# Kernel tuning notes

Measured on AMD Instinct MI355X. Metric: run time of the kernel, lower is better.

Reference implementation:

```python
import jax, jax.numpy as jnp
import numpy as np

KEEP_RATIO = 0.3
ALPHA, BETA, GAMMA, SMOOTH = 0.3, 0.7, 1.33, 1e-6
LOVASZ_W = 0.2


def _bce_with_logits(x, t):
    # stable binary_cross_entropy_with_logits, reduction='none'
    return jnp.maximum(x, 0.0) - x * t + jnp.log1p(jnp.exp(-jnp.abs(x)))


def _ohem_image(loss_i, tgt_i, tis_i, k_all):
    # loss_i/tgt_i/tis_i: [P] per-image flattened
    P = loss_i.shape[0]
    pos = tgt_i * tis_i                       # 1.0 where kept positive
    n_pos = jnp.sum(pos).astype(jnp.int32)
    neg_mask = (tgt_i == 0) & (tis_i == 1)
    n_remain = jnp.maximum(0, k_all - n_pos)
    # top-n_remain negative losses via full descending sort + rank mask
    neg_vals = jnp.where(neg_mask, loss_i, -jnp.inf)
    neg_sorted = -jnp.sort(-neg_vals)         # descending
    ranks = jnp.arange(P)
    valid = (ranks < n_remain) & jnp.isfinite(neg_sorted)
    neg_sum = jnp.sum(jnp.where(valid, neg_sorted, 0.0))
    n_neg_kept = jnp.sum(valid).astype(jnp.int32)
    pos_sum = jnp.sum(loss_i * pos)
    cnt = n_pos + n_neg_kept
    # fallback when nothing kept: hardest pixel inside tissue (or pixel 0)
    tis_vals = jnp.where(tis_i == 1, loss_i, -jnp.inf)
    has_tissue = jnp.any(tis_i == 1)
    fallback = jnp.where(has_tissue, jnp.max(tis_vals), loss_i[0])
    return jnp.where(cnt > 0, (pos_sum + neg_sum) / jnp.maximum(cnt, 1), fallback)


def _lovasz_image(log_flat, lab_flat):
    # binary Lovasz hinge, per image
    signs = 2.0 * lab_flat - 1.0
    errors = 1.0 - log_flat * signs
    order = jnp.argsort(-errors)              # descending by error
    errors_sorted = errors[order]
    gt_sorted = lab_flat[order]
    p = jnp.sum(gt_sorted)
    intersection = p - jnp.cumsum(gt_sorted)
    union = p + jnp.cumsum(1.0 - gt_sorted)
    jaccard = 1.0 - intersection / union
    n = gt_sorted.shape[0] - p
    grad = jnp.where(n > 0,
                     jnp.concatenate([jaccard[:1], jaccard[1:] - jaccard[:-1]]),
                     jaccard)
    return jnp.dot(jax.nn.relu(errors_sorted), grad)


def _forward(logits, targets, tissue_mask):
    t = targets.astype(jnp.float32)
    B = logits.shape[0]
    lf = logits.reshape(B, -1)                # [B, P]
    tf = t.reshape(B, -1)
    mf = tissue_mask.reshape(B, -1)
    P = lf.shape[1]
    k_all = max(1, int(P * KEEP_RATIO))       # static

    # --- OHEM BCE ---
    bce = _bce_with_logits(lf, tf) * mf
    ohem_i = jax.vmap(lambda l, tg, ms: _ohem_image(l, tg, ms, k_all))(bce, tf, mf)
    ohem_term = jnp.mean(ohem_i)

    # --- focal Tversky (per image) ---
    probs = jax.nn.sigmoid(lf)
    tp = jnp.sum(probs * tf, axis=1)
    fn = jnp.sum((1.0 - probs) * tf, axis=1)
    fp = jnp.sum(probs * (1.0 - tf), axis=1)
    tversky = (tp + SMOOTH) / (tp + ALPHA * fn + BETA * fp + SMOOTH)
    ft_i = (1.0 - tversky) ** GAMMA

    # --- Lovasz hinge (per image) ---
    lov_i = jax.vmap(_lovasz_image)(lf, tf)

    # masked mean over images that contain positives
    posb = jnp.sum(tf, axis=1) > 0
    npos = jnp.sum(posb)
    denom = jnp.maximum(npos, 1).astype(lf.dtype)
    ft_term = jnp.sum(jnp.where(posb, ft_i, 0.0)) / denom
    lov_term = jnp.sum(jnp.where(posb, lov_i, 0.0)) / denom
    return ohem_term + jnp.where(npos > 0, ft_term + LOVASZ_W * lov_term, 0.0)


def setup_inputs() -> dict:
    key = jax.random.key(0)
    k1, k2 = jax.random.split(key)
    B, H, W = 16, 768, 768
    logits = jax.random.normal(k1, (B, 1, H, W), dtype=jnp.float32)
    targets = jax.random.randint(k2, (B, 1, H, W), 0, 2, dtype=jnp.int32)
    tissue_mask = jnp.ones((B, 1, H, W), dtype=jnp.float32)
    return {"logits": logits, "targets": targets, "tissue_mask": tissue_mask}


def reference(logits, targets, tissue_mask):
    return _forward(logits, targets, tissue_mask)
```

## Files before the change

### kernel.cpp

```cpp
#include <hip/hip_runtime.h>
#include <math.h>

#define BB 16
#define PP (768*768)
#define NBINS 4096
#define CHUNKS 96
#define KALL 176947

#define LOV_LO (-17.0f)
#define LOV_RANGE 34.0f

typedef unsigned long long u64;

struct PAcc { float pos_sum, pos_w, tpx, sprx, mx, sum_t, n_tis, bce0; };
struct AccR { float lov_i, ft_i, ohem_i; unsigned posb; };

__device__ inline float wred_sum(float v) {
  #pragma unroll
  for (int o = 32; o > 0; o >>= 1) v += __shfl_down(v, o, 64);
  return v;
}
__device__ inline float wred_max(float v) {
  #pragma unroll
  for (int o = 32; o > 0; o >>= 1) v = fmaxf(v, __shfl_down(v, o, 64));
  return v;
}

__global__ __launch_bounds__(256) void k_main(const float* __restrict__ logits,
                                              const int* __restrict__ targets,
                                              const float* __restrict__ mask,
                                              PAcc* __restrict__ pacc,
                                              unsigned* __restrict__ partial1,
                                              unsigned* __restrict__ partial3)
{
  const int b = blockIdx.y;
  const int chunk = blockIdx.x;
  __shared__ unsigned hist1[NBINS];
  __shared__ unsigned hist3p[NBINS / 2];
  __shared__ float wsum[4][8];
  for (int i = threadIdx.x; i < NBINS; i += 256) hist1[i] = 0u;
  for (int i = threadIdx.x; i < NBINS / 2; i += 256) hist3p[i] = 0u;
  __syncthreads();

  const float4* l4 = (const float4*)(logits + (size_t)b * PP);
  const int4*   t4 = (const int4*)(targets + (size_t)b * PP);
  const float4* m4 = (const float4*)(mask + (size_t)b * PP);

  const float lov_scale = (float)NBINS / LOV_RANGE;

  float pos_sum = 0.f, pos_w = 0.f, tpa = 0.f, spra = 0.f, mx = 0.f;
  float sum_t = 0.f, n_tis = 0.f, bce0 = 0.f;

  if (chunk == 0 && threadIdx.x == 0) {
    float l = logits[(size_t)b * PP];
    float tf = (float)targets[(size_t)b * PP];
    float m = mask[(size_t)b * PP];
    float ex = __expf(-fabsf(l));
    bce0 = (fmaxf(l, 0.f) + __logf(1.f + ex) - l * tf) * m;
  }

  const int per_chunk4 = (PP / CHUNKS) / 4;
  const int base4 = chunk * per_chunk4;
  const int iters = per_chunk4 / 256;

  for (int it = 0; it < iters; ++it) {
    int i = base4 + it * 256 + threadIdx.x;
    float4 lv = l4[i]; int4 tv = t4[i]; float4 mv = m4[i];
    float ls[4] = {lv.x, lv.y, lv.z, lv.w};
    int   ts[4] = {tv.x, tv.y, tv.z, tv.w};
    float ms[4] = {mv.x, mv.y, mv.z, mv.w};
    #pragma unroll
    for (int c = 0; c < 4; ++c) {
      float l = ls[c]; int ti = ts[c]; float tf = (float)ti; float m = ms[c];
      float ex = __expf(-fabsf(l));
      float lg = __logf(1.f + ex);
      float loss = (fmaxf(l, 0.f) + lg - l * tf) * m;
      float posw = tf * m;
      pos_sum = fmaf(loss, posw, pos_sum);
      pos_w  += posw;
      float pr = ((l >= 0.f) ? 1.f : ex) * __builtin_amdgcn_rcpf(1.f + ex);
      spra += pr;
      tpa = fmaf(pr, tf, tpa);
      sum_t += tf;
      bool tis = (m == 1.0f);
      if (tis) { n_tis += 1.f; mx = fmaxf(mx, loss); }
      float s = fmaf(2.f, tf, -1.f);
      float e = fmaf(-l, s, 1.f);
      int bin = (int)((e - LOV_LO) * lov_scale);
      bin = bin < 0 ? 0 : (bin > NBINS - 1 ? NBINS - 1 : bin);
      atomicAdd(&hist1[bin], 1u | ((unsigned)ti << 16));
      if ((ti == 0) & !tis)
        atomicAdd(&hist3p[bin >> 1], 1u << ((bin & 1) << 4));
    }
  }

  {
    float v0 = wred_sum(pos_sum), v1 = wred_sum(pos_w), v2 = wred_sum(tpa);
    float v3 = wred_sum(spra), v4 = wred_max(mx), v5 = wred_sum(sum_t);
    float v6 = wred_sum(n_tis), v7 = wred_sum(bce0);
    int w = threadIdx.x >> 6, lane = threadIdx.x & 63;
    if (lane == 0) {
      wsum[w][0] = v0; wsum[w][1] = v1; wsum[w][2] = v2; wsum[w][3] = v3;
      wsum[w][4] = v4; wsum[w][5] = v5; wsum[w][6] = v6; wsum[w][7] = v7;
    }
  }
  __syncthreads();
  if (threadIdx.x == 0) {
    PAcc r;
    r.pos_sum = wsum[0][0] + wsum[1][0] + wsum[2][0] + wsum[3][0];
    r.pos_w   = wsum[0][1] + wsum[1][1] + wsum[2][1] + wsum[3][1];
    r.tpx     = wsum[0][2] + wsum[1][2] + wsum[2][2] + wsum[3][2];
    r.sprx    = wsum[0][3] + wsum[1][3] + wsum[2][3] + wsum[3][3];
    r.mx      = fmaxf(fmaxf(wsum[0][4], wsum[1][4]), fmaxf(wsum[2][4], wsum[3][4]));
    r.sum_t   = wsum[0][5] + wsum[1][5] + wsum[2][5] + wsum[3][5];
    r.n_tis   = wsum[0][6] + wsum[1][6] + wsum[2][6] + wsum[3][6];
    r.bce0    = wsum[0][7] + wsum[1][7] + wsum[2][7] + wsum[3][7];
    pacc[(size_t)b * CHUNKS + chunk] = r;
  }

  {
    unsigned* d1 = partial1 + ((size_t)b * CHUNKS + chunk) * NBINS;
    for (int i = threadIdx.x; i < NBINS; i += 256) d1[i] = hist1[i];
    unsigned* d3 = partial3 + ((size_t)b * CHUNKS + chunk) * (NBINS / 2);
    for (int i = threadIdx.x; i < NBINS / 2; i += 256) d3[i] = hist3p[i];
  }
}

__global__ __launch_bounds__(256) void k_reduce(const unsigned* __restrict__ partial1,
                                                const unsigned* __restrict__ partial3,
                                                u64* __restrict__ ghist,
                                                const PAcc* __restrict__ pacc,
                                                PAcc* __restrict__ accImg,
                                                unsigned* __restrict__ ticket)
{
  const int img = blockIdx.y;
  const int slice = blockIdx.x;
  const int bin = slice * 256 + threadIdx.x;
  const unsigned* s1 = partial1 + (size_t)img * CHUNKS * NBINS + bin;
  const unsigned* s3 = partial3 + (size_t)img * CHUNKS * (NBINS / 2) + (bin >> 1);
  const unsigned sh3 = (bin & 1) << 4;
  unsigned c = 0, q = 0, n0 = 0;
  #pragma unroll 4
  for (int p = 0; p < CHUNKS; ++p) {
    unsigned v = s1[(size_t)p * NBINS];
    c += v & 0xFFFFu; q += v >> 16;
    n0 += (s3[(size_t)p * (NBINS / 2)] >> sh3) & 0xFFFFu;
  }
  unsigned negtis = (c - q) - n0;
  ghist[(size_t)img * NBINS + bin] =
      (u64)c | ((u64)q << 20) | ((u64)negtis << 40);

  if (slice == 0 && threadIdx.x < 128) {
    int t = threadIdx.x;
    PAcc v;
    if (t < CHUNKS) v = pacc[(size_t)img * CHUNKS + t];
    else { v.pos_sum = v.pos_w = v.tpx = v.sprx = v.mx = v.sum_t = v.n_tis = v.bce0 = 0.f; }
    v.pos_sum = wred_sum(v.pos_sum); v.pos_w = wred_sum(v.pos_w);
    v.tpx = wred_sum(v.tpx); v.sprx = wred_sum(v.sprx);
    v.mx = wred_max(v.mx); v.sum_t = wred_sum(v.sum_t);
    v.n_tis = wred_sum(v.n_tis); v.bce0 = wred_sum(v.bce0);
    __shared__ PAcc half[2];
    if ((t & 63) == 0) half[t >> 6] = v;
    __syncthreads();
    if (t == 0) {
      PAcc r = half[0], h = half[1];
      r.pos_sum += h.pos_sum; r.pos_w += h.pos_w; r.tpx += h.tpx; r.sprx += h.sprx;
      r.mx = fmaxf(r.mx, h.mx); r.sum_t += h.sum_t; r.n_tis += h.n_tis; r.bce0 += h.bce0;
      accImg[img] = r;
    }
  }
  if (slice == 0 && img == 0 && threadIdx.x == 0) *ticket = 0u;
}

__global__ __launch_bounds__(256) void k_scan(const PAcc* __restrict__ accImg,
                                              const u64* __restrict__ ghist,
                                              AccR* __restrict__ acc,
                                              unsigned* __restrict__ ticket,
                                              float* __restrict__ out)
{
  const int b = blockIdx.x;
  const int t = threadIdx.x;
  __shared__ unsigned sA[256], sB[256], sC[256];
  __shared__ float sf[256], sg[256];
  __shared__ unsigned ng_total_sh;

  const u64* gh = ghist + (size_t)b * NBINS;
  const PAcc a = accImg[b];

  const unsigned sum_t = (unsigned)a.sum_t;
  const float p = (float)sum_t;
  const bool has_pos = sum_t > 0;
  const unsigned n_neg_total = (unsigned)PP - sum_t;
  const int CH = NBINS / 256;
  const float lov_d = LOV_RANGE / (float)NBINS;

  int n_pos = (int)a.pos_w;
  int n_remain = KALL - n_pos; if (n_remain < 0) n_remain = 0;

  u64 loc[16];
  unsigned tc = 0, tq = 0, tn = 0;
  #pragma unroll
  for (int k = 0; k < 16; ++k) {
    u64 v = gh[NBINS - 1 - (t * CH + k)];
    loc[k] = v;
    tc += (unsigned)(v & 0xFFFFFu);
    tq += (unsigned)((v >> 20) & 0xFFFFFu);
    tn += (unsigned)((v >> 40) & 0xFFFFFu);
  }
  sA[t] = tc; sB[t] = tq; sC[t] = tn;
  __syncthreads();
  if (t == 0) {
    unsigned aI = 0, aC = 0, aN = 0;
    for (int i = 0; i < 256; i++) {
      unsigned ci = sA[i], qi = sB[i], ni = sC[i];
      sA[i] = aI; sB[i] = aC; sC[i] = aN;
      aI += ci; aC += qi; aN += ni;
    }
    ng_total_sh = aN;
  }
  __syncthreads();

  float lov_local = 0.f, ns_local = 0.f;
  {
    unsigned I = sA[t], C = sB[t], NG = sC[t];
    float Jprev = has_pos ? (1.f - (p - (float)C) / (p + (float)I - (float)C)) : 0.f;
    #pragma unroll 4
    for (int k = 0; k < 16; ++k) {
      int j = NBINS - 1 - (t * CH + k);
      u64 v = loc[k];
      unsigned c = (unsigned)(v & 0xFFFFFu);
      if (c) {
        unsigned q = (unsigned)((v >> 20) & 0xFFFFFu);
        unsigned ng = (unsigned)((v >> 40) & 0xFFFFFu);
        float e = LOV_LO + ((float)j + 0.5f) * lov_d;
        if (has_pos) {
          float re = fmaxf(e, 0.f);
          if (n_neg_total > 0) {
            I += c; C += q;
            float Jb = 1.f - (p - (float)C) / (p + (float)I - (float)C);
            lov_local += re * (Jb - Jprev);
            Jprev = Jb;
          } else {
            double hi = (double)I + (double)c;
            double s = (hi * (hi + 1.0) - (double)I * ((double)I + 1.0)) * 0.5 / (double)p;
            lov_local += re * (float)s;
            I += c;
          }
        }
        if (n_remain > 0 && ng) {
          long long rem = (long long)n_remain - (long long)NG;
          unsigned take = rem <= 0 ? 0u : (rem >= (long long)ng ? ng : (unsigned)rem);
          if (take) {
            float l = e - 1.f;
            float nloss = fmaxf(l, 0.f) + __logf(1.f + __expf(-fabsf(l)));
            ns_local += (float)take * nloss;
          }
          NG += ng;
        }
      }
    }
  }
  sf[t] = lov_local; sg[t] = ns_local; __syncthreads();
  for (int off = 128; off > 0; off >>= 1) {
    if (t < off) { sf[t] += sf[t + off]; sg[t] += sg[t + off]; }
    __syncthreads();
  }

  if (t == 0) {
    float lov = sf[0];
    float neg_sum = sg[0];
    unsigned kept = (n_remain > 0)
        ? ((unsigned)n_remain < ng_total_sh ? (unsigned)n_remain : ng_total_sh) : 0u;
    float cnt = (float)n_pos + (float)kept;
    float ohem;
    if (cnt > 0.f) ohem = (a.pos_sum + neg_sum) / cnt;
    else ohem = (a.n_tis > 0.f) ? a.mx : a.bce0;
    float tp = a.tpx;
    float fn = p - tp;
    float fp = a.sprx - tp;
    float tv = (tp + 1e-6f) / (tp + 0.3f * fn + 0.7f * fp + 1e-6f);
    float ft = powf(fmaxf(1.f - tv, 0.f), 1.33f);
    acc[b].lov_i = lov; acc[b].ft_i = ft; acc[b].ohem_i = ohem;
    acc[b].posb = has_pos ? 1u : 0u;

    __threadfence();
    unsigned ret = atomicAdd(ticket, 1u);
    if (ret == BB - 1) {
      __threadfence();
      volatile AccR* va = acc;
      float os = 0.f, fts = 0.f, lvs = 0.f; int np = 0;
      for (int i = 0; i < BB; i++) {
        os += va[i].ohem_i;
        if (va[i].posb) { np++; fts += va[i].ft_i; lvs += va[i].lov_i; }
      }
      float denom = (np > 0) ? (float)np : 1.f;
      float r = os / (float)BB;
      if (np > 0) r += fts / denom + 0.2f * (lvs / denom);
      out[0] = r;
    }
  }
}

extern "C" void kernel_launch(void* const* d_in, const int* in_sizes, int n_in,
                              void* d_out, int out_size, void* d_ws, size_t ws_size,
                              hipStream_t stream) {
  const float* logits  = (const float*)d_in[0];
  const int*   targets = (const int*)d_in[1];
  const float* mask    = (const float*)d_in[2];
  float* out = (float*)d_out;

  char* ws = (char*)d_ws;
  AccR*     acc      = (AccR*)ws;
  unsigned* ticket   = (unsigned*)(ws + 256);
  PAcc*     accImg   = (PAcc*)(ws + 512);
  PAcc*     pacc     = (PAcc*)(ws + 1024);
  u64*      ghist    = (u64*)(ws + (64 << 10));
  unsigned* partial1 = (unsigned*)(ws + (1 << 20));
  unsigned* partial3 = (unsigned*)(ws + (1 << 20) + (size_t)BB * CHUNKS * NBINS * 4);
  (void)in_sizes; (void)n_in; (void)out_size; (void)ws_size;


  dim3 g1(CHUNKS, BB, 1);
  k_main<<<g1, 256, 0, stream>>>(logits, targets, mask, pacc, partial1, partial3);
  dim3 g2(NBINS / 256, BB, 1);
  k_reduce<<<g2, 256, 0, stream>>>(partial1, partial3, ghist, pacc, accImg, ticket);
  k_scan<<<BB, 256, 0, stream>>>(accImg, ghist, acc, ticket, out);
}
```

Baseline: 170.9 us.

## Fuse reduce and scan kernels, skip unused negative-tissue histograms

Merges the reduce and scan kernels into one tail kernel. A per-image ticket picks the last slice block to run the scan, which removes one launch and the gap between them. k_main now writes a per-chunk flag saying whether any non-tissue pixels exist. It skips storing hist3p when the flag is clear, and the tail kernel skips reading it. It also unrolls the main loop two float4 groups at a time and adds an occupancy hint to launch_bounds. The cost is more ticket and fence synchronisation, and extra register pressure from the wider loads.

After: 198.0 us. +15.9%, slower.

```diff
diff --git a/kernel.cpp b/kernel.cpp
--- a/kernel.cpp
+++ b/kernel.cpp
@@ -5,6 +5,7 @@
 #define PP (768*768)
 #define NBINS 4096
 #define CHUNKS 96
+#define PIXB (PP / CHUNKS)
 #define KALL 176947
 
 #define LOV_LO (-17.0f)
@@ -26,20 +27,24 @@
   return v;
 }
 
-__global__ __launch_bounds__(256) void k_main(const float* __restrict__ logits,
-                                              const int* __restrict__ targets,
-                                              const float* __restrict__ mask,
-                                              PAcc* __restrict__ pacc,
-                                              unsigned* __restrict__ partial1,
-                                              unsigned* __restrict__ partial3)
+__global__ __launch_bounds__(256, 6) void k_main(const float* __restrict__ logits,
+                                                 const int* __restrict__ targets,
+                                                 const float* __restrict__ mask,
+                                                 PAcc* __restrict__ pacc,
+                                                 unsigned* __restrict__ partial1,
+                                                 unsigned* __restrict__ partial3,
+                                                 unsigned* __restrict__ flags,
+                                                 unsigned* __restrict__ tickets)
 {
   const int b = blockIdx.y;
   const int chunk = blockIdx.x;
   __shared__ unsigned hist1[NBINS];
   __shared__ unsigned hist3p[NBINS / 2];
   __shared__ float wsum[4][8];
+  __shared__ unsigned s_any3;
   for (int i = threadIdx.x; i < NBINS; i += 256) hist1[i] = 0u;
   for (int i = threadIdx.x; i < NBINS / 2; i += 256) hist3p[i] = 0u;
+  if (b == 0 && chunk == 0 && threadIdx.x < 17) tickets[threadIdx.x] = 0u;
   __syncthreads();
 
   const float4* l4 = (const float4*)(logits + (size_t)b * PP);
@@ -59,39 +64,45 @@
     bce0 = (fmaxf(l, 0.f) + __logf(1.f + ex) - l * tf) * m;
   }
 
-  const int per_chunk4 = (PP / CHUNKS) / 4;
+  auto px = [&](float l, int ti, float m) {
+    float tf = (float)ti;
+    float ex = __expf(-fabsf(l));
+    float lg = __logf(1.f + ex);
+    float loss = (fmaxf(l, 0.f) + lg - l * tf) * m;
+    float posw = tf * m;
+    pos_sum = fmaf(loss, posw, pos_sum);
+    pos_w  += posw;
+    float pr = ((l >= 0.f) ? 1.f : ex) * __builtin_amdgcn_rcpf(1.f + ex);
+    spra += pr;
+    tpa = fmaf(pr, tf, tpa);
+    sum_t += tf;
+    bool tis = (m == 1.0f);
+    if (tis) { n_tis += 1.f; mx = fmaxf(mx, loss); }
+    float s = fmaf(2.f, tf, -1.f);
+    float e = fmaf(-l, s, 1.f);
+    int bin = (int)((e - LOV_LO) * lov_scale);
+    bin = bin < 0 ? 0 : (bin > NBINS - 1 ? NBINS - 1 : bin);
+    atomicAdd(&hist1[bin], 1u | ((unsigned)ti << 16));
+    if ((ti == 0) & !tis)
+      atomicAdd(&hist3p[bin >> 1], 1u << ((bin & 1) << 4));
+  };
+  auto grp = [&](float4 lv, int4 tv, float4 mv) {
+    px(lv.x, tv.x, mv.x); px(lv.y, tv.y, mv.y);
+    px(lv.z, tv.z, mv.z); px(lv.w, tv.w, mv.w);
+  };
+
+  const int per_chunk4 = PIXB / 4;
   const int base4 = chunk * per_chunk4;
   const int iters = per_chunk4 / 256;
 
-  for (int it = 0; it < iters; ++it) {
-    int i = base4 + it * 256 + threadIdx.x;
-    float4 lv = l4[i]; int4 tv = t4[i]; float4 mv = m4[i];
-    float ls[4] = {lv.x, lv.y, lv.z, lv.w};
-    int   ts[4] = {tv.x, tv.y, tv.z, tv.w};
-    float ms[4] = {mv.x, mv.y, mv.z, mv.w};
-    #pragma unroll
-    for (int c = 0; c < 4; ++c) {
-      float l = ls[c]; int ti = ts[c]; float tf = (float)ti; float m = ms[c];
-      float ex = __expf(-fabsf(l));
-      float lg = __logf(1.f + ex);
-      float loss = (fmaxf(l, 0.f) + lg - l * tf) * m;
-      float posw = tf * m;
-      pos_sum = fmaf(loss, posw, pos_sum);
-      pos_w  += posw;
-      float pr = ((l >= 0.f) ? 1.f : ex) * __builtin_amdgcn_rcpf(1.f + ex);
-      spra += pr;
-      tpa = fmaf(pr, tf, tpa);
-      sum_t += tf;
-      bool tis = (m == 1.0f);
-      if (tis) { n_tis += 1.f; mx = fmaxf(mx, loss); }
-      float s = fmaf(2.f, tf, -1.f);
-      float e = fmaf(-l, s, 1.f);
-      int bin = (int)((e - LOV_LO) * lov_scale);
-      bin = bin < 0 ? 0 : (bin > NBINS - 1 ? NBINS - 1 : bin);
-      atomicAdd(&hist1[bin], 1u | ((unsigned)ti << 16));
-      if ((ti == 0) & !tis)
-        atomicAdd(&hist3p[bin >> 1], 1u << ((bin & 1) << 4));
-    }
+  for (int it = 0; it < iters; it += 2) {
+    int ia = base4 + it * 256 + threadIdx.x;
+    int ib = ia + 256;
+    float4 lva = l4[ia]; float4 lvb = l4[ib];
+    int4   tva = t4[ia]; int4   tvb = t4[ib];
+    float4 mva = m4[ia]; float4 mvb = m4[ib];
+    grp(lva, tva, mva);
+    grp(lvb, tvb, mvb);
   }
 
   {
@@ -116,76 +127,90 @@
     r.n_tis   = wsum[0][6] + wsum[1][6] + wsum[2][6] + wsum[3][6];
     r.bce0    = wsum[0][7] + wsum[1][7] + wsum[2][7] + wsum[3][7];
     pacc[(size_t)b * CHUNKS + chunk] = r;
-  }
+    unsigned any3 = (r.n_tis != (float)PIXB) ? 1u : 0u;
+    s_any3 = any3;
+    flags[(size_t)b * CHUNKS + chunk] = any3;
+  }
+  __syncthreads();
 
   {
     unsigned* d1 = partial1 + ((size_t)b * CHUNKS + chunk) * NBINS;
     for (int i = threadIdx.x; i < NBINS; i += 256) d1[i] = hist1[i];
-    unsigned* d3 = partial3 + ((size_t)b * CHUNKS + chunk) * (NBINS / 2);
-    for (int i = threadIdx.x; i < NBINS / 2; i += 256) d3[i] = hist3p[i];
-  }
-}
-
-__global__ __launch_bounds__(256) void k_reduce(const unsigned* __restrict__ partial1,
-                                                const unsigned* __restrict__ partial3,
-                                                u64* __restrict__ ghist,
-                                                const PAcc* __restrict__ pacc,
-                                                PAcc* __restrict__ accImg,
-                                                unsigned* __restrict__ ticket)
+    if (s_any3) {
+      unsigned* d3 = partial3 + ((size_t)b * CHUNKS + chunk) * (NBINS / 2);
+      for (int i = threadIdx.x; i < NBINS / 2; i += 256) d3[i] = hist3p[i];
+    }
+  }
+}
+
+__global__ __launch_bounds__(256) void k_tail(const unsigned* __restrict__ partial1,
+                                              const unsigned* __restrict__ partial3,
+                                              const unsigned* __restrict__ flags,
+                                              u64* __restrict__ ghist,
+                                              const PAcc* __restrict__ pacc,
+                                              PAcc* __restrict__ accImg,
+                                              AccR* __restrict__ acc,
+                                              unsigned* __restrict__ tickets,
+                                              float* __restrict__ out)
 {
   const int img = blockIdx.y;
   const int slice = blockIdx.x;
-  const int bin = slice * 256 + threadIdx.x;
-  const unsigned* s1 = partial1 + (size_t)img * CHUNKS * NBINS + bin;
-  const unsigned* s3 = partial3 + (size_t)img * CHUNKS * (NBINS / 2) + (bin >> 1);
-  const unsigned sh3 = (bin & 1) << 4;
-  unsigned c = 0, q = 0, n0 = 0;
-  #pragma unroll 4
-  for (int p = 0; p < CHUNKS; ++p) {
-    unsigned v = s1[(size_t)p * NBINS];
-    c += v & 0xFFFFu; q += v >> 16;
-    n0 += (s3[(size_t)p * (NBINS / 2)] >> sh3) & 0xFFFFu;
-  }
-  unsigned negtis = (c - q) - n0;
-  ghist[(size_t)img * NBINS + bin] =
-      (u64)c | ((u64)q << 20) | ((u64)negtis << 40);
-
-  if (slice == 0 && threadIdx.x < 128) {
-    int t = threadIdx.x;
+  const int t = threadIdx.x;
+  __shared__ unsigned sA[256], sB[256], sC[256];
+  __shared__ float sf[256], sg[256];
+  __shared__ unsigned s_flags[CHUNKS];
+  __shared__ PAcc half[2];
+  __shared__ unsigned s_do, ng_total_sh;
+
+  if (t < CHUNKS) s_flags[t] = flags[(size_t)img * CHUNKS + t];
+  __syncthreads();
+
+  {
+    const int bin = slice * 256 + t;
+    const unsigned* s1 = partial1 + (size_t)img * CHUNKS * NBINS + bin;
+    const unsigned* s3 = partial3 + (size_t)img * CHUNKS * (NBINS / 2) + (bin >> 1);
+    const unsigned sh3 = (bin & 1) << 4;
+    unsigned c = 0, q = 0, n0 = 0;
+    #pragma unroll 4
+    for (int p = 0; p < CHUNKS; ++p) {
+      unsigned v = s1[(size_t)p * NBINS];
+      c += v & 0xFFFFu; q += v >> 16;
+      if (s_flags[p]) n0 += (s3[(size_t)p * (NBINS / 2)] >> sh3) & 0xFFFFu;
+    }
+    unsigned negtis = (c - q) - n0;
+    ghist[(size_t)img * NBINS + bin] = (u64)c | ((u64)q << 20) | ((u64)negtis << 40);
+  }
+
+  {
     PAcc v;
-    if (t < CHUNKS) v = pacc[(size_t)img * CHUNKS + t];
-    else { v.pos_sum = v.pos_w = v.tpx = v.sprx = v.mx = v.sum_t = v.n_tis = v.bce0 = 0.f; }
+    v.pos_sum = v.pos_w = v.tpx = v.sprx = v.mx = v.sum_t = v.n_tis = v.bce0 = 0.f;
+    if (slice == 0 && t < CHUNKS) v = pacc[(size_t)img * CHUNKS + t];
     v.pos_sum = wred_sum(v.pos_sum); v.pos_w = wred_sum(v.pos_w);
     v.tpx = wred_sum(v.tpx); v.sprx = wred_sum(v.sprx);
     v.mx = wred_max(v.mx); v.sum_t = wred_sum(v.sum_t);
     v.n_tis = wred_sum(v.n_tis); v.bce0 = wred_sum(v.bce0);
-    __shared__ PAcc half[2];
-    if ((t & 63) == 0) half[t >> 6] = v;
+    if (t < 128 && (t & 63) == 0) half[t >> 6] = v;
     __syncthreads();
-    if (t == 0) {
+    if (slice == 0 && t == 0) {
       PAcc r = half[0], h = half[1];
       r.pos_sum += h.pos_sum; r.pos_w += h.pos_w; r.tpx += h.tpx; r.sprx += h.sprx;
       r.mx = fmaxf(r.mx, h.mx); r.sum_t += h.sum_t; r.n_tis += h.n_tis; r.bce0 += h.bce0;
       accImg[img] = r;
     }
   }
-  if (slice == 0 && img == 0 && threadIdx.x == 0) *ticket = 0u;
-}
-
-__global__ __launch_bounds__(256) void k_scan(const PAcc* __restrict__ accImg,
-                                              const u64* __restrict__ ghist,
-                                              AccR* __restrict__ acc,
-                                              unsigned* __restrict__ ticket,
-                                              float* __restrict__ out)
-{
-  const int b = blockIdx.x;
-  const int t = threadIdx.x;
-  __shared__ unsigned sA[256], sB[256], sC[256];
-  __shared__ float sf[256], sg[256];
-  __shared__ unsigned ng_total_sh;
-
-  const u64* gh = ghist + (size_t)b * NBINS;
-  const PAcc a = accImg[b];
+
+  __threadfence();
+  __syncthreads();
+  if (t == 0) {
+    unsigned ret = atomicAdd(&tickets[img], 1u);
+    s_do = (ret == (unsigned)(NBINS / 256) - 1) ? 1u : 0u;
+  }
+  __syncthreads();
+  if (!s_do) return;
+  __threadfence();
+
+  const u64* gh = ghist + (size_t)img * NBINS;
+  const PAcc a = accImg[img];
 
   const unsigned sum_t = (unsigned)a.sum_t;
   const float p = (float)sum_t;
@@ -280,12 +305,12 @@
     float fp = a.sprx - tp;
     float tv = (tp + 1e-6f) / (tp + 0.3f * fn + 0.7f * fp + 1e-6f);
     float ft = powf(fmaxf(1.f - tv, 0.f), 1.33f);
-    acc[b].lov_i = lov; acc[b].ft_i = ft; acc[b].ohem_i = ohem;
-    acc[b].posb = has_pos ? 1u : 0u;
+    acc[img].lov_i = lov; acc[img].ft_i = ft; acc[img].ohem_i = ohem;
+    acc[img].posb = has_pos ? 1u : 0u;
 
     __threadfence();
-    unsigned ret = atomicAdd(ticket, 1u);
-    if (ret == BB - 1) {
+    unsigned ret2 = atomicAdd(&tickets[16], 1u);
+    if (ret2 == BB - 1) {
       __threadfence();
       volatile AccR* va = acc;
       float os = 0.f, fts = 0.f, lvs = 0.f; int np = 0;
@@ -311,18 +336,19 @@
 
   char* ws = (char*)d_ws;
   AccR*     acc      = (AccR*)ws;
-  unsigned* ticket   = (unsigned*)(ws + 256);
+  unsigned* tickets  = (unsigned*)(ws + 256);
   PAcc*     accImg   = (PAcc*)(ws + 512);
   PAcc*     pacc     = (PAcc*)(ws + 1024);
-  u64*      ghist    = (u64*)(ws + (64 << 10));
+  unsigned* flags    = (unsigned*)(ws + (64 << 10));
+  u64*      ghist    = (u64*)(ws + (128 << 10));
   unsigned* partial1 = (unsigned*)(ws + (1 << 20));
   unsigned* partial3 = (unsigned*)(ws + (1 << 20) + (size_t)BB * CHUNKS * NBINS * 4);
   (void)in_sizes; (void)n_in; (void)out_size; (void)ws_size;
 
-
   dim3 g1(CHUNKS, BB, 1);
-  k_main<<<g1, 256, 0, stream>>>(logits, targets, mask, pacc, partial1, partial3);
+  k_main<<<g1, 256, 0, stream>>>(logits, targets, mask, pacc, partial1, partial3,
+                                 flags, tickets);
   dim3 g2(NBINS / 256, BB, 1);
-  k_reduce<<<g2, 256, 0, stream>>>(partial1, partial3, ghist, pacc, accImg, ticket);
-  k_scan<<<BB, 256, 0, stream>>>(accImg, ghist, acc, ticket, out);
-}
+  k_tail<<<g2, 256, 0, stream>>>(partial1, partial3, flags, ghist, pacc, accImg,
+                                 acc, tickets, out);
+}
```
